# Performance work log

Hardware: AMD Instinct MI355X
Metric: run time of the kernel (lower is better)

## Reference

```python
import jax, jax.numpy as jnp
import numpy as np

# Predictive-coding graph message passing (PCGraphConv core compute).
# Single-graph edge list (edge_src -> edge_dst) with one scalar weight per edge,
# tiled over the batch (weights.repeat(1, batchsize) in the original).
# PredictionMessagePassing: mu_i = sum_{e: dst(e)=i} w_e * f(x_{src(e)})
# ValueMessagePassing:      dx_j = -eps_j + f'(x_j) * sum_{e: src(e)=j} w_e * eps_{dst(e)}
# with eps = x - mu and f = tanh.

N_PER_GRAPH = 4096
E_PER_GRAPH = 524288
BATCH = 32


def setup_inputs() -> dict:
    key = jax.random.key(0)
    k1, k2, k3, k4 = jax.random.split(key, 4)
    x = jax.random.normal(k1, (BATCH * N_PER_GRAPH,), dtype=jnp.float32)
    weights = jax.random.normal(k2, (E_PER_GRAPH,), dtype=jnp.float32) * (1.0 / np.sqrt(N_PER_GRAPH))
    edge_src = jax.random.randint(k3, (E_PER_GRAPH,), 0, N_PER_GRAPH, dtype=jnp.int32)
    edge_dst = jax.random.randint(k4, (E_PER_GRAPH,), 0, N_PER_GRAPH, dtype=jnp.int32)
    return {"x": x, "weights": weights, "edge_src": edge_src, "edge_dst": edge_dst,
            "batch_size": BATCH, "num_vertices": N_PER_GRAPH}


def reference(x, weights, edge_src, edge_dst, batch_size, num_vertices):
    B, N = batch_size, num_vertices
    BN = B * N
    # Tile single-graph edges across the batch with per-graph node offsets.
    offs = (jnp.arange(B, dtype=edge_src.dtype) * N)[:, None]        # [B,1]
    src = (edge_src[None, :] + offs).reshape(-1)                     # [B*E]
    dst = (edge_dst[None, :] + offs).reshape(-1)                     # [B*E]
    w = jnp.tile(weights, B)                                         # [B*E]

    fx = jnp.tanh(x)                                                 # f(x)
    # Predictions: gather f(x) at src, weight per edge, scatter-add at dst.
    mu = jax.ops.segment_sum(w * fx[src], dst, num_segments=BN)      # [B*N]
    eps = x - mu                                                     # errors
    fprime = 1.0 - fx * fx                                           # f'(x)
    # Value update: backward flow of errors along edges.
    dx = -eps + fprime * jax.ops.segment_sum(w * eps[dst], src, num_segments=BN)
    return jnp.stack([mu, dx])                                       # [2, B*N]
```

## Files before the change

kernel.cpp:

```cpp
#include <hip/hip_runtime.h>


static constexpr int kB = 32, kLogB = 5;
static constexpr int kTileNodes = 8;
static constexpr int kNumBins = 512;
static constexpr int kCap = 1408;
static constexpr int kChunk = 2048;

__global__ void __launch_bounds__(256) k_init(
    const float* __restrict__ x, float* __restrict__ x_t,
    float* __restrict__ fx_t, int* __restrict__ cursA, int* __restrict__ cursB,
    int N) {
  __shared__ float tile[32][65];
  int tid = threadIdx.x;
  int n0 = blockIdx.x * 64;
  if (blockIdx.x == 0) {
    for (int t = tid; t < kNumBins; t += 256) { cursA[t] = 0; cursB[t] = 0; }
  }
  for (int k = tid; k < 32 * 64; k += 256) {
    int b = k >> 6, n = k & 63;
    tile[b][n] = x[b * N + n0 + n];
  }
  __syncthreads();
  for (int k = tid; k < 64 * 32; k += 256) {
    int n = k >> 5, b = k & 31;
    float xv = tile[b][n];
    int j = (n0 + n) * kB + b;
    x_t[j] = xv;
    fx_t[j] = tanhf(xv);
  }
}

__global__ void __launch_bounds__(256) k_bin_dual(
    const int* __restrict__ esrc, const int* __restrict__ edst,
    const float* __restrict__ w, uint2* __restrict__ binsA,
    uint2* __restrict__ binsB, int* __restrict__ cursA,
    int* __restrict__ cursB, int E) {
  __shared__ int histA[kNumBins], histB[kNumBins];
  __shared__ int baseA[kNumBins], baseB[kNumBins];
  __shared__ unsigned short lsrc[kChunk], ldst[kChunk];
  __shared__ unsigned short loffA[kChunk], loffB[kChunk];
  int tid = threadIdx.x;
  int e0 = blockIdx.x * kChunk;
  int nloc = min(kChunk, E - e0);
  for (int t = tid; t < kNumBins; t += 256) { histA[t] = 0; histB[t] = 0; }
  __syncthreads();
  for (int k = tid; k < nloc; k += 256) {
    int s = esrc[e0 + k], d = edst[e0 + k];
    lsrc[k] = (unsigned short)s;
    ldst[k] = (unsigned short)d;
    loffA[k] = (unsigned short)atomicAdd(&histA[d >> 3], 1);
    loffB[k] = (unsigned short)atomicAdd(&histB[s >> 3], 1);
  }
  __syncthreads();
  for (int t = tid; t < kNumBins; t += 256) {
    baseA[t] = atomicAdd(&cursA[t], histA[t]);
    baseB[t] = atomicAdd(&cursB[t], histB[t]);
  }
  __syncthreads();
  for (int k = tid; k < nloc; k += 256) {
    float wv = w[e0 + k];
    unsigned wu = __float_as_uint(wv);
    int s = lsrc[k], d = ldst[k];
    int binA = d >> 3, posA = baseA[binA] + loffA[k];
    if (posA < kCap)
      binsA[(size_t)binA * kCap + posA] = make_uint2(((unsigned)s << 8) | (d & 7), wu);
    int binB = s >> 3, posB = baseB[binB] + loffB[k];
    if (posB < kCap)
      binsB[(size_t)binB * kCap + posB] = make_uint2(((unsigned)d << 8) | (s & 7), wu);
  }
}

__global__ void __launch_bounds__(1024) k_accum(
    const uint2* __restrict__ bins, const int* __restrict__ cursors,
    const float* __restrict__ vals, const float* __restrict__ x_t,
    const float* __restrict__ fx_t, const float* __restrict__ eps_in,
    float* __restrict__ o1, float* __restrict__ o2, int mode) {
  __shared__ float acc[32][kTileNodes * kB];
  int tid = threadIdx.x;
  int b = tid & 31;
  int slot = tid >> 5;
  float* my = acc[slot];
#pragma unroll
  for (int l = 0; l < kTileNodes; l++) my[l * kB + b] = 0.0f;
  int t = blockIdx.x;
  int cnt = min(cursors[t], kCap);
  const uint2* bp = bins + (size_t)t * kCap;

  int i = slot;
  uint2 r0 = (i < cnt) ? bp[i] : make_uint2(0u, 0u);
  uint2 r1 = (i + 32 < cnt) ? bp[i + 32] : make_uint2(0u, 0u);
  float v0 = (i < cnt) ? vals[((r0.x >> 8) << kLogB) + b] : 0.0f;
  while (i < cnt) {
    uint2 r2 = (i + 64 < cnt) ? bp[i + 64] : make_uint2(0u, 0u);
    float v1 = (i + 32 < cnt) ? vals[((r1.x >> 8) << kLogB) + b] : 0.0f;
    my[(r0.x & 7) * kB + b] += __uint_as_float(r0.y) * v0;
    r0 = r1; r1 = r2; v0 = v1;
    i += 32;
  }
  __syncthreads();
  if (tid < kTileNodes * kB) {
    int local = tid >> 5, bb = tid & 31;
    float s = 0.0f;
#pragma unroll
    for (int sl = 0; sl < 32; sl++) s += acc[sl][local * kB + bb];
    int j = (t * kTileNodes + local) * kB + bb;
    if (mode == 0) {
      o1[j] = s;
      o2[j] = x_t[j] - s;
    } else {
      float fx = fx_t[j];
      o1[j] = fmaf(1.0f - fx * fx, s, -eps_in[j]);
    }
  }
}

__global__ void __launch_bounds__(256) k_final(
    const float* __restrict__ mu_t, const float* __restrict__ dx_t,
    float* __restrict__ out_mu, float* __restrict__ out_dx, int N) {
  __shared__ float tile[64][33];
  int tid = threadIdx.x;
  int nblk = N >> 6;
  int which = blockIdx.x / nblk;
  int n0 = (blockIdx.x % nblk) * 64;
  const float* src = which ? dx_t : mu_t;
  float* dst = which ? out_dx : out_mu;
  for (int k = tid; k < 64 * 32; k += 256) {
    int n = k >> 5, b = k & 31;
    tile[n][b] = src[(n0 + n) * kB + b];
  }
  __syncthreads();
  for (int k = tid; k < 32 * 64; k += 256) {
    int b = k >> 6, n = k & 63;
    dst[b * N + n0 + n] = tile[n][b];
  }
}

extern "C" void kernel_launch(void* const* d_in, const int* in_sizes, int n_in,
                              void* d_out, int out_size, void* d_ws, size_t ws_size,
                              hipStream_t stream) {
  const float* x    = (const float*)d_in[0];
  const float* w    = (const float*)d_in[1];
  const int*   esrc = (const int*)d_in[2];
  const int*   edst = (const int*)d_in[3];

  const int BN = in_sizes[0];
  const int E  = in_sizes[1];
  const int N  = BN / kB;

  float* ws    = (float*)d_ws;
  float* x_t   = ws;
  float* fx_t  = ws + (size_t)BN;
  float* eps_t = ws + 2 * (size_t)BN;
  float* mu_t  = ws + 3 * (size_t)BN;
  float* dx_t  = ws + 4 * (size_t)BN;
  int*   cursA = (int*)(ws + 5 * (size_t)BN);
  int*   cursB = cursA + kNumBins;
  uint2* binsA = (uint2*)(cursB + kNumBins);
  uint2* binsB = binsA + (size_t)kNumBins * kCap;

  float* out_mu = (float*)d_out;
  float* out_dx = (float*)d_out + BN;

  int nblk_bin = (E + kChunk - 1) / kChunk;

  k_init<<<N / 64, 256, 0, stream>>>(x, x_t, fx_t, cursA, cursB, N);
  k_bin_dual<<<nblk_bin, 256, 0, stream>>>(esrc, edst, w, binsA, binsB,
                                           cursA, cursB, E);
  k_accum<<<kNumBins, 1024, 0, stream>>>(binsA, cursA, fx_t, x_t, fx_t, fx_t,
                                         mu_t, eps_t, 0);
  k_accum<<<kNumBins, 1024, 0, stream>>>(binsB, cursB, eps_t, x_t, fx_t, eps_t,
                                         dx_t, dx_t, 1);
  k_final<<<2 * (N / 64), 256, 0, stream>>>(mu_t, dx_t, out_mu, out_dx, N);
}
```

Measured before the change: 120.1 us.

## Fuse output transpose into accumulation kernels and restructure edge binning

Removes the separate transpose kernel by having each accumulation block write its results directly to the batch-major output, padding the shared accumulator rows to 33 so the transposed reduction reads avoid bank conflicts. Binning now uses 1024-thread blocks that keep the edges and their local offsets in registers instead of shared memory. Cursor zeroing moves from the init kernel to a memset, and the gather loop prefetches one more stage ahead. The direct output writes are strided by N across batch lanes, so they coalesce worse than the old tiled transpose did.

```diff
diff --git a/kernel.cpp b/kernel.cpp
--- a/kernel.cpp
+++ b/kernel.cpp
@@ -6,17 +6,14 @@
 static constexpr int kNumBins = 512;
 static constexpr int kCap = 1408;
 static constexpr int kChunk = 2048;
+static constexpr int kRowPad = 33;
 
 __global__ void __launch_bounds__(256) k_init(
     const float* __restrict__ x, float* __restrict__ x_t,
-    float* __restrict__ fx_t, int* __restrict__ cursA, int* __restrict__ cursB,
-    int N) {
+    float* __restrict__ fx_t, int N) {
   __shared__ float tile[32][65];
   int tid = threadIdx.x;
   int n0 = blockIdx.x * 64;
-  if (blockIdx.x == 0) {
-    for (int t = tid; t < kNumBins; t += 256) { cursA[t] = 0; cursB[t] = 0; }
-  }
   for (int k = tid; k < 32 * 64; k += 256) {
     int b = k >> 6, n = k & 63;
     tile[b][n] = x[b * N + n0 + n];
@@ -31,108 +28,102 @@
   }
 }
 
-__global__ void __launch_bounds__(256) k_bin_dual(
+__global__ void __launch_bounds__(1024) k_bin_dual(
     const int* __restrict__ esrc, const int* __restrict__ edst,
     const float* __restrict__ w, uint2* __restrict__ binsA,
     uint2* __restrict__ binsB, int* __restrict__ cursA,
     int* __restrict__ cursB, int E) {
   __shared__ int histA[kNumBins], histB[kNumBins];
   __shared__ int baseA[kNumBins], baseB[kNumBins];
-  __shared__ unsigned short lsrc[kChunk], ldst[kChunk];
-  __shared__ unsigned short loffA[kChunk], loffB[kChunk];
   int tid = threadIdx.x;
   int e0 = blockIdx.x * kChunk;
   int nloc = min(kChunk, E - e0);
-  for (int t = tid; t < kNumBins; t += 256) { histA[t] = 0; histB[t] = 0; }
+  if (tid < kNumBins) { histA[tid] = 0; histB[tid] = 0; }
   __syncthreads();
-  for (int k = tid; k < nloc; k += 256) {
-    int s = esrc[e0 + k], d = edst[e0 + k];
-    lsrc[k] = (unsigned short)s;
-    ldst[k] = (unsigned short)d;
-    loffA[k] = (unsigned short)atomicAdd(&histA[d >> 3], 1);
-    loffB[k] = (unsigned short)atomicAdd(&histB[s >> 3], 1);
+  int k0 = tid, k1 = tid + 1024;
+  int s0 = 0, d0 = 0, s1 = 0, d1 = 0;
+  unsigned lA0 = 0, lB0 = 0, lA1 = 0, lB1 = 0;
+  bool has0 = k0 < nloc, has1 = k1 < nloc;
+  if (has0) {
+    s0 = esrc[e0 + k0]; d0 = edst[e0 + k0];
+    lA0 = atomicAdd(&histA[d0 >> 3], 1);
+    lB0 = atomicAdd(&histB[s0 >> 3], 1);
+  }
+  if (has1) {
+    s1 = esrc[e0 + k1]; d1 = edst[e0 + k1];
+    lA1 = atomicAdd(&histA[d1 >> 3], 1);
+    lB1 = atomicAdd(&histB[s1 >> 3], 1);
   }
   __syncthreads();
-  for (int t = tid; t < kNumBins; t += 256) {
-    baseA[t] = atomicAdd(&cursA[t], histA[t]);
-    baseB[t] = atomicAdd(&cursB[t], histB[t]);
+  if (tid < kNumBins) {
+    baseA[tid] = atomicAdd(&cursA[tid], histA[tid]);
+    baseB[tid] = atomicAdd(&cursB[tid], histB[tid]);
   }
   __syncthreads();
-  for (int k = tid; k < nloc; k += 256) {
-    float wv = w[e0 + k];
-    unsigned wu = __float_as_uint(wv);
-    int s = lsrc[k], d = ldst[k];
-    int binA = d >> 3, posA = baseA[binA] + loffA[k];
+  if (has0) {
+    unsigned wu = __float_as_uint(w[e0 + k0]);
+    int binA = d0 >> 3; int posA = baseA[binA] + (int)lA0;
     if (posA < kCap)
-      binsA[(size_t)binA * kCap + posA] = make_uint2(((unsigned)s << 8) | (d & 7), wu);
-    int binB = s >> 3, posB = baseB[binB] + loffB[k];
+      binsA[(size_t)binA * kCap + posA] = make_uint2(((unsigned)s0 << 8) | (d0 & 7), wu);
+    int binB = s0 >> 3; int posB = baseB[binB] + (int)lB0;
     if (posB < kCap)
-      binsB[(size_t)binB * kCap + posB] = make_uint2(((unsigned)d << 8) | (s & 7), wu);
+      binsB[(size_t)binB * kCap + posB] = make_uint2(((unsigned)d0 << 8) | (s0 & 7), wu);
+  }
+  if (has1) {
+    unsigned wu = __float_as_uint(w[e0 + k1]);
+    int binA = d1 >> 3; int posA = baseA[binA] + (int)lA1;
+    if (posA < kCap)
+      binsA[(size_t)binA * kCap + posA] = make_uint2(((unsigned)s1 << 8) | (d1 & 7), wu);
+    int binB = s1 >> 3; int posB = baseB[binB] + (int)lB1;
+    if (posB < kCap)
+      binsB[(size_t)binB * kCap + posB] = make_uint2(((unsigned)d1 << 8) | (s1 & 7), wu);
   }
 }
 
 __global__ void __launch_bounds__(1024) k_accum(
     const uint2* __restrict__ bins, const int* __restrict__ cursors,
     const float* __restrict__ vals, const float* __restrict__ x_t,
-    const float* __restrict__ fx_t, const float* __restrict__ eps_in,
-    float* __restrict__ o1, float* __restrict__ o2, int mode) {
-  __shared__ float acc[32][kTileNodes * kB];
+    const float* __restrict__ fx_t, float* __restrict__ eps_t,
+    float* __restrict__ out, int N, int mode) {
+  __shared__ float acc[32][kTileNodes * kRowPad];
   int tid = threadIdx.x;
   int b = tid & 31;
   int slot = tid >> 5;
   float* my = acc[slot];
 #pragma unroll
-  for (int l = 0; l < kTileNodes; l++) my[l * kB + b] = 0.0f;
+  for (int l = 0; l < kTileNodes; l++) my[l * kRowPad + b] = 0.0f;
   int t = blockIdx.x;
   int cnt = min(cursors[t], kCap);
   const uint2* bp = bins + (size_t)t * kCap;
 
   int i = slot;
-  uint2 r0 = (i < cnt) ? bp[i] : make_uint2(0u, 0u);
+  uint2 r0 = (i      < cnt) ? bp[i]      : make_uint2(0u, 0u);
   uint2 r1 = (i + 32 < cnt) ? bp[i + 32] : make_uint2(0u, 0u);
-  float v0 = (i < cnt) ? vals[((r0.x >> 8) << kLogB) + b] : 0.0f;
+  uint2 r2 = (i + 64 < cnt) ? bp[i + 64] : make_uint2(0u, 0u);
+  float v0 = (i      < cnt) ? vals[((r0.x >> 8) << kLogB) + b] : 0.0f;
+  float v1 = (i + 32 < cnt) ? vals[((r1.x >> 8) << kLogB) + b] : 0.0f;
   while (i < cnt) {
-    uint2 r2 = (i + 64 < cnt) ? bp[i + 64] : make_uint2(0u, 0u);
-    float v1 = (i + 32 < cnt) ? vals[((r1.x >> 8) << kLogB) + b] : 0.0f;
-    my[(r0.x & 7) * kB + b] += __uint_as_float(r0.y) * v0;
-    r0 = r1; r1 = r2; v0 = v1;
+    uint2 r3 = (i + 96 < cnt) ? bp[i + 96] : make_uint2(0u, 0u);
+    float v2 = (i + 64 < cnt) ? vals[((r2.x >> 8) << kLogB) + b] : 0.0f;
+    my[(r0.x & 7) * kRowPad + b] += __uint_as_float(r0.y) * v0;
+    r0 = r1; r1 = r2; r2 = r3; v0 = v1; v1 = v2;
     i += 32;
   }
   __syncthreads();
   if (tid < kTileNodes * kB) {
-    int local = tid >> 5, bb = tid & 31;
+    int local = tid & 7, bb = tid >> 3;
     float s = 0.0f;
 #pragma unroll
-    for (int sl = 0; sl < 32; sl++) s += acc[sl][local * kB + bb];
-    int j = (t * kTileNodes + local) * kB + bb;
+    for (int sl = 0; sl < 32; sl++) s += acc[sl][local * kRowPad + bb];
+    int n = t * kTileNodes + local;
+    int j = n * kB + bb;
     if (mode == 0) {
-      o1[j] = s;
-      o2[j] = x_t[j] - s;
+      out[bb * N + n] = s;
+      eps_t[j] = x_t[j] - s;
     } else {
       float fx = fx_t[j];
-      o1[j] = fmaf(1.0f - fx * fx, s, -eps_in[j]);
+      out[bb * N + n] = fmaf(1.0f - fx * fx, s, -eps_t[j]);
     }
-  }
-}
-
-__global__ void __launch_bounds__(256) k_final(
-    const float* __restrict__ mu_t, const float* __restrict__ dx_t,
-    float* __restrict__ out_mu, float* __restrict__ out_dx, int N) {
-  __shared__ float tile[64][33];
-  int tid = threadIdx.x;
-  int nblk = N >> 6;
-  int which = blockIdx.x / nblk;
-  int n0 = (blockIdx.x % nblk) * 64;
-  const float* src = which ? dx_t : mu_t;
-  float* dst = which ? out_dx : out_mu;
-  for (int k = tid; k < 64 * 32; k += 256) {
-    int n = k >> 5, b = k & 31;
-    tile[n][b] = src[(n0 + n) * kB + b];
-  }
-  __syncthreads();
-  for (int k = tid; k < 32 * 64; k += 256) {
-    int b = k >> 6, n = k & 63;
-    dst[b * N + n0 + n] = tile[n][b];
   }
 }
 
@@ -152,9 +143,7 @@
   float* x_t   = ws;
   float* fx_t  = ws + (size_t)BN;
   float* eps_t = ws + 2 * (size_t)BN;
-  float* mu_t  = ws + 3 * (size_t)BN;
-  float* dx_t  = ws + 4 * (size_t)BN;
-  int*   cursA = (int*)(ws + 5 * (size_t)BN);
+  int*   cursA = (int*)(ws + 3 * (size_t)BN);
   int*   cursB = cursA + kNumBins;
   uint2* binsA = (uint2*)(cursB + kNumBins);
   uint2* binsB = binsA + (size_t)kNumBins * kCap;
@@ -164,12 +153,12 @@
 
   int nblk_bin = (E + kChunk - 1) / kChunk;
 
-  k_init<<<N / 64, 256, 0, stream>>>(x, x_t, fx_t, cursA, cursB, N);
-  k_bin_dual<<<nblk_bin, 256, 0, stream>>>(esrc, edst, w, binsA, binsB,
-                                           cursA, cursB, E);
-  k_accum<<<kNumBins, 1024, 0, stream>>>(binsA, cursA, fx_t, x_t, fx_t, fx_t,
-                                         mu_t, eps_t, 0);
-  k_accum<<<kNumBins, 1024, 0, stream>>>(binsB, cursB, eps_t, x_t, fx_t, eps_t,
-                                         dx_t, dx_t, 1);
-  k_final<<<2 * (N / 64), 256, 0, stream>>>(mu_t, dx_t, out_mu, out_dx, N);
+  hipMemsetAsync(cursA, 0, 2 * kNumBins * sizeof(int), stream);
+  k_init<<<N / 64, 256, 0, stream>>>(x, x_t, fx_t, N);
+  k_bin_dual<<<nblk_bin, 1024, 0, stream>>>(esrc, edst, w, binsA, binsB,
+                                            cursA, cursB, E);
+  k_accum<<<kNumBins, 1024, 0, stream>>>(binsA, cursA, fx_t, x_t, fx_t,
+                                         eps_t, out_mu, N, 0);
+  k_accum<<<kNumBins, 1024, 0, stream>>>(binsB, cursB, eps_t, x_t, fx_t,
+                                         eps_t, out_dx, N, 1);
 }
```

Measured after the change: 116.4 us. 3.1% less time.
